# Kernel tuning notes

Hardware: AMD Instinct MI355X
Metric: run time of the kernel (lower is better)

The kernel has to match this reference:

```python
import jax, jax.numpy as jnp
import numpy as np

N_NODES = 20000
N_EDGES = 8192
UNITS = 128
NUM_GAUSSIANS = 50
CUTOFF = 8.0
GAMMA = 10.0
MIN_DIST, MAX_DIST = 0.0, 30.0


def setup_inputs() -> dict:
    key = jax.random.key(0)
    ks = jax.random.split(key, 6)
    node_features = jax.random.normal(ks[0], (N_NODES, UNITS), dtype=jnp.float32)
    edge_indices = jax.random.randint(ks[1], (2, N_EDGES), 0, N_NODES, dtype=jnp.int32)
    distances = jax.random.uniform(ks[2], (N_EDGES,), dtype=jnp.float32)
    # filter network params (Dense(units) -> swish -> Dense(units*units))
    W1 = jax.random.normal(ks[3], (NUM_GAUSSIANS, UNITS), dtype=jnp.float32) / np.sqrt(NUM_GAUSSIANS)
    b1 = jnp.zeros((UNITS,), dtype=jnp.float32)
    W2 = jax.random.normal(ks[4], (UNITS, UNITS * UNITS), dtype=jnp.float32) / np.sqrt(UNITS)
    b2 = jnp.zeros((UNITS * UNITS,), dtype=jnp.float32)
    # transform Dense(units, use_bias=False)
    Wt = jax.random.normal(ks[5], (UNITS, UNITS), dtype=jnp.float32) / np.sqrt(UNITS)
    return {"node_features": node_features, "edge_indices": edge_indices,
            "distances": distances, "W1": W1, "b1": b1, "W2": W2, "b2": b2, "Wt": Wt}


def reference(node_features, edge_indices, distances, W1, b1, W2, b2, Wt):
    n_nodes, units = node_features.shape
    # cutoff mask (multiplicative; dropped edges contribute zero to the scatter-sum,
    # equivalent to tf.boolean_mask + unsorted_segment_sum)
    mask = (distances <= CUTOFF).astype(node_features.dtype)  # [E]
    # Gaussian basis expansion
    centers = jnp.linspace(MIN_DIST, MAX_DIST, NUM_GAUSSIANS, dtype=jnp.float32)
    df = jnp.exp(-GAMMA * jnp.square(distances[:, None] - centers[None, :]))  # [E, G]
    # filter network: Dense -> swish -> Dense(units*units)
    h = jax.nn.silu(df @ W1 + b1)                    # [E, U]
    filters = (h @ W2 + b2).reshape(-1, units, units)  # [E, U, U]
    # gather source node features, transform, per-edge matvec
    src = node_features[edge_indices[0]]             # [E, U]
    transformed = src @ Wt                           # [E, U]
    filtered = jnp.einsum('eij,ej->ei', filters, transformed) * mask[:, None]  # [E, U]
    # scatter-sum to destination nodes
    messages = jax.ops.segment_sum(filtered, edge_indices[1], num_segments=n_nodes)
    return jax.nn.silu(messages)
```

## Files before the change

kernel.cpp:

```cpp
#include <hip/hip_runtime.h>
#include <hip/hip_fp16.h>


typedef _Float16 f16;
typedef __attribute__((ext_vector_type(8))) f16 f16x8;
typedef __attribute__((ext_vector_type(4))) float f32x4;
typedef __attribute__((ext_vector_type(4))) unsigned int u32x4;

#define NEDGE 8192
#define NNODE 20000
#define NG    50
#define KSTEPS 516
#define W2C_BYTES (KSTEPS * 8192)
#define HT_BYTES (64 * 132 * 128 * 2)
#define TM_BYTES (NEDGE * 128 * 2)
#define FP_BYTES ((size_t)NEDGE * 8 * 128 * 4)

#define LDS_H   0
#define LDS_TM  5120
#define LDS_TOT 37888

#define K_SRC 0
#define K_DF  16384
#define K_MSK 24576
#define K_WTC 24832
#define K_W1C 57600
#define K_TOT 73984

static __device__ __forceinline__ float fsilu(float x) { return x / (1.0f + __expf(-x)); }

static __device__ __forceinline__ void gll16(const void* g, void* l) {
  __builtin_amdgcn_global_load_lds(
      (const __attribute__((address_space(1))) unsigned int*)g,
      (__attribute__((address_space(3))) unsigned int*)l, 16, 0, 0);
}

__global__ __launch_bounds__(256) void kpre(const float* __restrict__ W2,
                                            const float* __restrict__ b2,
                                            const float* __restrict__ W1,
                                            const float* __restrict__ B1,
                                            const float* __restrict__ WT,
                                            const float* __restrict__ NF,
                                            const int*   __restrict__ EI,
                                            const float* __restrict__ DI,
                                            f16* __restrict__ w2c,
                                            f16* __restrict__ ht2,
                                            f16* __restrict__ tmo,
                                            float* __restrict__ out, int nz4) {
  __shared__ u32x4 smem_v[K_TOT / 16];
  char* smem = (char*)smem_v;
  const int bid = blockIdx.x, tid = threadIdx.x;

  if (bid < 516) {
    const int u = bid >> 2, s = bid & 3;
    const int i = tid >> 1, half = tid & 1;
    const float* src = ((u < 128) ? (W2 + (size_t)u * 16384) : b2)
                       + i * 128 + s * 32 + half * 16;
    union { f16 s16[16]; u32x4 v[2]; } pk;
#pragma unroll
    for (int q = 0; q < 4; ++q) {
      f32x4 v = *(const f32x4*)(src + q * 4);
#pragma unroll
      for (int r = 0; r < 4; ++r) pk.s16[q * 4 + r] = (f16)v[r];
    }
    const int nt = i >> 4, l15 = i & 15;
    u32x4* dst = (u32x4*)w2c + (size_t)(u * 4 + s) * 512 + nt * 64 + l15;
    dst[(half * 2 + 0) * 16] = pk.v[0];
    dst[(half * 2 + 1) * 16] = pk.v[1];
    return;
  }
  if (bid < 644) {
    const int bid2 = bid - 516;
    const int e0g = bid2 * 64;
    const int eb  = bid2 >> 1;
    const int el0 = (bid2 & 1) * 64;

#pragma unroll
    for (int q = 0; q < 8; ++q) {
      int f = q * 256 + tid;
      int lane = f & 63, nt = (f >> 6) & 7, step = f >> 9;
      int j = nt * 16 + (lane & 15);
      int u0 = step * 32 + (lane >> 4) * 8;
      union { f16 s[8]; u32x4 v; } pk;
#pragma unroll
      for (int r = 0; r < 8; ++r) pk.s[r] = (f16)WT[(u0 + r) * 128 + j];
      *(u32x4*)(smem + K_WTC + f * 16) = pk.v;
    }
#pragma unroll
    for (int q = 0; q < 4; ++q) {
      int f = q * 256 + tid;
      int lane = f & 63, nt = (f >> 6) & 7, step = f >> 9;
      int j = nt * 16 + (lane & 15);
      union { f16 s[8]; u32x4 v; } pk;
#pragma unroll
      for (int r = 0; r < 8; ++r) {
        int g = step * 32 + (lane >> 4) * 8 + r;
        float v = (g < 50) ? W1[g * 128 + j] : ((g == 63) ? B1[j] : 0.0f);
        pk.s[r] = (f16)v;
      }
      *(u32x4*)(smem + K_W1C + f * 16) = pk.v;
    }
    if (tid < 64) {
      float d = DI[e0g + tid];
      *(float*)(smem + K_MSK + tid * 4) = (d <= 8.0f) ? 1.0f : 0.0f;
    }
    {
      int e = tid >> 2, g0 = (tid & 3) * 16;
      float d = DI[e0g + e];
      union { f16 s[16]; u32x4 v[2]; } pk;
#pragma unroll
      for (int gg = 0; gg < 16; ++gg) {
        int g = g0 + gg;
        float x = d - (float)g * (30.0f / 49.0f);
        float v = (g < 50) ? __expf(-10.0f * x * x) : ((g == 63) ? 1.0f : 0.0f);
        pk.s[gg] = (f16)v;
      }
      int base = e * 128 + g0 * 2, sw = (e & 7) << 4;
      *(u32x4*)(smem + K_DF + ((base) ^ sw))      = pk.v[0];
      *(u32x4*)(smem + K_DF + ((base + 16) ^ sw)) = pk.v[1];
    }
#pragma unroll
    for (int p = 0; p < 8; ++p) {
      int e = p * 8 + (tid >> 5);
      int u0 = (tid & 31) * 4;
      int row = EI[e0g + e];
      f32x4 v = *(const f32x4*)(NF + (size_t)row * 128 + u0);
      union { f16 s[4]; unsigned long long q; } pk;
#pragma unroll
      for (int r = 0; r < 4; ++r) pk.s[r] = (f16)v[r];
      int addr = e * 256 + u0 * 2;
      *(unsigned long long*)(smem + K_SRC + (addr ^ ((e & 7) << 4))) = pk.q;
    }
    __syncthreads();

    const int w = tid >> 6, lane = tid & 63;
    const int l15 = lane & 15, g4 = lane >> 4;
    const int erow = w * 16;
    const int asw = (l15 & 7) << 4;

    f32x4 at[8], ah[8];
#pragma unroll
    for (int nt = 0; nt < 8; ++nt) {
      at[nt] = (f32x4){0.f, 0.f, 0.f, 0.f};
      ah[nt] = (f32x4){0.f, 0.f, 0.f, 0.f};
    }
#pragma unroll
    for (int step = 0; step < 4; ++step) {
      int aaddr = (erow + l15) * 256 + step * 64 + g4 * 16;
      f16x8 a = *(const f16x8*)(smem + K_SRC + (aaddr ^ asw));
#pragma unroll
      for (int nt = 0; nt < 8; ++nt) {
        f16x8 b = *(const f16x8*)(smem + K_WTC + ((step * 8 + nt) * 64 + lane) * 16);
        at[nt] = __builtin_amdgcn_mfma_f32_16x16x32_f16(a, b, at[nt], 0, 0, 0);
      }
    }
#pragma unroll
    for (int step = 0; step < 2; ++step) {
      int aaddr = (erow + l15) * 128 + step * 64 + g4 * 16;
      f16x8 a = *(const f16x8*)(smem + K_DF + (aaddr ^ asw));
#pragma unroll
      for (int nt = 0; nt < 8; ++nt) {
        f16x8 b = *(const f16x8*)(smem + K_W1C + ((step * 8 + nt) * 64 + lane) * 16);
        ah[nt] = __builtin_amdgcn_mfma_f32_16x16x32_f16(a, b, ah[nt], 0, 0, 0);
      }
    }
    const float* mk = (const float*)(smem + K_MSK);
#pragma unroll
    for (int r = 0; r < 4; ++r) {
      int el_ = erow + g4 * 4 + r;
      float m = mk[el_];
      int sw2 = (el_ & 7) << 4;
      char* rowp = (char*)tmo + (size_t)(e0g + el_) * 256;
#pragma unroll
      for (int nt = 0; nt < 8; ++nt)
        *(f16*)(rowp + (((nt * 16 + l15) * 2) ^ sw2)) = (f16)(m * at[nt][r]);
    }
#pragma unroll
    for (int r = 0; r < 4; ++r) {
      int el_ = el0 + erow + g4 * 4 + r;
#pragma unroll
      for (int nt = 0; nt < 8; ++nt) {
        int u = nt * 16 + l15;
        ht2[((size_t)eb * 132 + u) * 128 + el_] = (f16)fsilu(ah[nt][r]);
      }
    }
    if (tid < 64) ht2[((size_t)eb * 132 + 128) * 128 + el0 + tid] = (f16)1.0f;
    return;
  }
  {
    int base = (bid - 644) * 1024;
    f32x4 z = {0.f, 0.f, 0.f, 0.f};
#pragma unroll
    for (int k = 0; k < 4; ++k) {
      int i4 = base + k * 256 + tid;
      if (i4 < nz4) ((f32x4*)out)[i4] = z;
    }
  }
}

template<int MODE>
__global__ __launch_bounds__(256, 2) void k2_gemm(const f16* __restrict__ w2c,
                                                  const f16* __restrict__ ht2,
                                                  const f16* __restrict__ tm,
                                                  const int* __restrict__ EI,
                                                  float* __restrict__ fpart,
                                                  float* __restrict__ msg) {
  __shared__ u32x4 smem_v[LDS_TOT / 16];
  char* smem = (char*)smem_v;

  const int bid = blockIdx.x;
  const int c   = bid & 7;
  const int eb  = bid >> 3;
  const int e0  = eb * 128;
  const int nu  = (c == 7) ? 17 : 16;
  const int tid = threadIdx.x, w = tid >> 6, lane = tid & 63;
  const int l15 = lane & 15, g4 = lane >> 4;
  const int wm = w >> 1, wn = w & 1;

  const char* bp = (const char*)w2c + (size_t)(c * 64) * 8192 + wn * 4096 + lane * 16;
  f16x8 B0[4], B1[4];
#pragma unroll
  for (int nt = 0; nt < 4; ++nt) B0[nt] = *(const f16x8*)(bp + nt * 1024);
#pragma unroll
  for (int nt = 0; nt < 4; ++nt) B1[nt] = *(const f16x8*)(bp + 8192 + nt * 1024);

  {
    const char* tsrc = (const char*)tm + (size_t)e0 * 256 + w * 8192;
#pragma unroll
    for (int q = 0; q < 8; ++q)
      gll16(tsrc + q * 1024 + lane * 16,
            smem + LDS_TM + w * 8192 + q * 1024 + lane * 16);
  }
  if (w == 0) {
    const char* hsrc = (const char*)ht2 + ((size_t)eb * 132 + c * 16) * 256;
#pragma unroll
    for (int q = 0; q < 5; ++q)
      gll16(hsrc + q * 1024 + lane * 16, smem + LDS_H + q * 1024 + lane * 16);
  }
  __syncthreads();

  f16x8 Tall[4][4];
  {
    const int tmrow = LDS_TM + (wm * 64 + l15) * 256;
    const int colsw = (l15 & 7) << 4;
#pragma unroll
    for (int rt = 0; rt < 4; ++rt)
#pragma unroll
      for (int jc = 0; jc < 4; ++jc)
        Tall[rt][jc] = *(const f16x8*)(smem + tmrow + rt * 4096 +
                                       ((jc * 64 + g4 * 16) ^ colsw));
  }
  const __half* hbase = (const __half*)(smem + LDS_H) + wm * 64 + l15;

  __half2 hc[4], hn[4];
#pragma unroll
  for (int rt = 0; rt < 4; ++rt) hc[rt] = __half2half2(hbase[rt * 16]);

  size_t off = 2 * 8192;
  f32x4 acc[4][4];
#pragma unroll
  for (int rt = 0; rt < 4; ++rt)
#pragma unroll
    for (int nt = 0; nt < 4; ++nt) acc[rt][nt] = (f32x4){0.f, 0.f, 0.f, 0.f};

  for (int u = 0; u < nu; ++u) {
#pragma unroll
    for (int jc = 0; jc < 4; ++jc) {
      if (jc == 1) {
#pragma unroll
        for (int rt = 0; rt < 4; ++rt)
          hn[rt] = __half2half2(hbase[(u + 1) * 128 + rt * 16]);
      }
      union uf { f16x8 v; __half2 h[4]; };
      uf a[4];
#pragma unroll
      for (int rt = 0; rt < 4; ++rt) {
        uf t; t.v = Tall[rt][jc];
#pragma unroll
        for (int q = 0; q < 4; ++q) a[rt].h[q] = __hmul2(t.h[q], hc[rt]);
      }
      __builtin_amdgcn_s_setprio(1);
#pragma unroll
      for (int nt = 0; nt < 4; ++nt) {
        if ((jc & 1) == 0) {
#pragma unroll
          for (int rt = 0; rt < 4; ++rt)
            acc[rt][nt] = __builtin_amdgcn_mfma_f32_16x16x32_f16(a[rt].v, B0[nt], acc[rt][nt], 0, 0, 0);
          B0[nt] = *(const f16x8*)(bp + off + nt * 1024);
        } else {
#pragma unroll
          for (int rt = 0; rt < 4; ++rt)
            acc[rt][nt] = __builtin_amdgcn_mfma_f32_16x16x32_f16(a[rt].v, B1[nt], acc[rt][nt], 0, 0, 0);
          B1[nt] = *(const f16x8*)(bp + off + nt * 1024);
        }
      }
      __builtin_amdgcn_s_setprio(0);
      off += 8192;
    }
#pragma unroll
    for (int rt = 0; rt < 4; ++rt) hc[rt] = hn[rt];
  }

  if (MODE == 0) {
#pragma unroll
    for (int rt = 0; rt < 4; ++rt) {
#pragma unroll
      for (int r = 0; r < 4; ++r) {
        int e = e0 + wm * 64 + rt * 16 + g4 * 4 + r;
        float* prow = fpart + ((size_t)e * 8 + c) * 128 + wn * 64 + l15;
#pragma unroll
        for (int nt = 0; nt < 4; ++nt)
          prow[nt * 16] = acc[rt][nt][r];
      }
    }
  } else {
    const int* dst = EI + NEDGE;
#pragma unroll
    for (int rt = 0; rt < 4; ++rt) {
#pragma unroll
      for (int r = 0; r < 4; ++r) {
        int e = e0 + wm * 64 + rt * 16 + g4 * 4 + r;
        float* row = msg + (size_t)dst[e] * 128 + wn * 64 + l15;
#pragma unroll
        for (int nt = 0; nt < 4; ++nt)
          atomicAdd(row + nt * 16, acc[rt][nt][r]);
      }
    }
  }
}

__global__ __launch_bounds__(256) void k4_reduce(const float* __restrict__ fp,
                                                 const int* __restrict__ EI,
                                                 float* __restrict__ out) {
  int gid = blockIdx.x * 256 + threadIdx.x;
  int e  = gid >> 5;
  int i0 = (gid & 31) << 2;
  const float* ep = fp + (size_t)e * 1024 + i0;
  f32x4 s = {0.f, 0.f, 0.f, 0.f};
#pragma unroll
  for (int cc = 0; cc < 8; ++cc) {
    f32x4 v = *(const f32x4*)(ep + cc * 128);
    s[0] += v[0]; s[1] += v[1]; s[2] += v[2]; s[3] += v[3];
  }
  float* row = out + (size_t)EI[NEDGE + e] * 128 + i0;
  atomicAdd(row + 0, s[0]);
  atomicAdd(row + 1, s[1]);
  atomicAdd(row + 2, s[2]);
  atomicAdd(row + 3, s[3]);
}

__global__ __launch_bounds__(256) void k3_silu(float* __restrict__ out, int n4) {
  int idx = blockIdx.x * 256 + threadIdx.x;
  int stride = gridDim.x * 256;
  f32x4* p = (f32x4*)out;
  for (; idx < n4; idx += stride) {
    f32x4 v = p[idx];
#pragma unroll
    for (int cc = 0; cc < 4; ++cc) v[cc] = fsilu(v[cc]);
    p[idx] = v;
  }
}

extern "C" void kernel_launch(void* const* d_in, const int* in_sizes, int n_in,
                              void* d_out, int out_size, void* d_ws, size_t ws_size,
                              hipStream_t stream) {
  const float* NF = (const float*)d_in[0];
  const int*   EI = (const int*)  d_in[1];
  const float* DI = (const float*)d_in[2];
  const float* W1 = (const float*)d_in[3];
  const float* B1 = (const float*)d_in[4];
  const float* W2 = (const float*)d_in[5];
  const float* B2 = (const float*)d_in[6];
  const float* WT = (const float*)d_in[7];
  float* out = (float*)d_out;

  char* base = (char*)d_ws;
  f16*   w2c = (f16*)base;
  f16*   ht2 = (f16*)(base + W2C_BYTES);
  f16*   tmo = (f16*)(base + W2C_BYTES + HT_BYTES);
  float* fp  = (float*)(base + W2C_BYTES + HT_BYTES + TM_BYTES);
  size_t need_min  = (size_t)W2C_BYTES + HT_BYTES + TM_BYTES;
  size_t need_fast = need_min + FP_BYTES;
  if (ws_size < need_min) return;
  const bool fast = (ws_size >= need_fast);

  int nz4 = out_size / 4;
  int zb  = (nz4 + 1023) / 1024;
  kpre<<<dim3(644 + zb), dim3(256), 0, stream>>>(W2, B2, W1, B1, WT, NF, EI, DI,
                                                 w2c, ht2, tmo, out, nz4);
  if (fast) {
    k2_gemm<0><<<dim3(512),  dim3(256), 0, stream>>>(w2c, ht2, tmo, EI, fp, out);
    k4_reduce <<<dim3(1024), dim3(256), 0, stream>>>(fp, EI, out);
  } else {
    k2_gemm<1><<<dim3(512),  dim3(256), 0, stream>>>(w2c, ht2, tmo, EI, fp, out);
  }
  k3_silu<<<dim3(1024), dim3(256), 0, stream>>>(out, nz4);
}
```

Measured before the change: 82.20 us.

## Fuse reduce and silu into GEMM kernel using grid-wide atomic barriers

Merges the partial-sum reduction kernel and the final silu kernel into the GEMM kernel. Phases are separated by a software grid barrier built on an atomic counter in the workspace, and the counter is reset by the preceding kernel. This removes two kernel launches and their launch gaps. It relies on all 512 blocks being co-resident (launch bounds of 2 blocks per CU on 256 CUs), and the spin-wait barriers add synchronisation cost and a deadlock risk if residency is not met.

```diff
diff --git a/kernel.cpp b/kernel.cpp
--- a/kernel.cpp
+++ b/kernel.cpp
@@ -14,6 +14,7 @@
 #define W2C_BYTES (KSTEPS * 8192)
 #define HT_BYTES (64 * 132 * 128 * 2)
 #define TM_BYTES (NEDGE * 128 * 2)
+#define CNT_BYTES 256
 #define FP_BYTES ((size_t)NEDGE * 8 * 128 * 4)
 
 #define LDS_H   0
@@ -33,6 +34,17 @@
   __builtin_amdgcn_global_load_lds(
       (const __attribute__((address_space(1))) unsigned int*)g,
       (__attribute__((address_space(3))) unsigned int*)l, 16, 0, 0);
+}
+
+static __device__ __forceinline__ void gbar(unsigned* cnt, unsigned target) {
+  __syncthreads();
+  if (threadIdx.x == 0) {
+    __threadfence();
+    __hip_atomic_fetch_add(cnt, 1u, __ATOMIC_ACQ_REL, __HIP_MEMORY_SCOPE_AGENT);
+    while (__hip_atomic_load(cnt, __ATOMIC_ACQUIRE, __HIP_MEMORY_SCOPE_AGENT) < target)
+      __builtin_amdgcn_s_sleep(8);
+  }
+  __syncthreads();
 }
 
 __global__ __launch_bounds__(256) void kpre(const float* __restrict__ W2,
@@ -46,7 +58,8 @@
                                             f16* __restrict__ w2c,
                                             f16* __restrict__ ht2,
                                             f16* __restrict__ tmo,
-                                            float* __restrict__ out, int nz4) {
+                                            float* __restrict__ out,
+                                            unsigned* __restrict__ cnt, int nz4) {
   __shared__ u32x4 smem_v[K_TOT / 16];
   char* smem = (char*)smem_v;
   const int bid = blockIdx.x, tid = threadIdx.x;
@@ -188,6 +201,7 @@
     return;
   }
   {
+    if (bid == 644 && tid == 0) *cnt = 0u;
     int base = (bid - 644) * 1024;
     f32x4 z = {0.f, 0.f, 0.f, 0.f};
 #pragma unroll
@@ -199,12 +213,13 @@
 }
 
 template<int MODE>
-__global__ __launch_bounds__(256, 2) void k2_gemm(const f16* __restrict__ w2c,
-                                                  const f16* __restrict__ ht2,
-                                                  const f16* __restrict__ tm,
-                                                  const int* __restrict__ EI,
-                                                  float* __restrict__ fpart,
-                                                  float* __restrict__ msg) {
+__global__ __launch_bounds__(256, 2) void k2f(const f16* __restrict__ w2c,
+                                              const f16* __restrict__ ht2,
+                                              const f16* __restrict__ tm,
+                                              const int* __restrict__ EI,
+                                              float* __restrict__ fpart,
+                                              float* __restrict__ out,
+                                              unsigned* __restrict__ cnt, int nz4) {
   __shared__ u32x4 smem_v[LDS_TOT / 16];
   char* smem = (char*)smem_v;
 
@@ -320,44 +335,49 @@
 #pragma unroll
       for (int r = 0; r < 4; ++r) {
         int e = e0 + wm * 64 + rt * 16 + g4 * 4 + r;
-        float* row = msg + (size_t)dst[e] * 128 + wn * 64 + l15;
+        float* row = out + (size_t)dst[e] * 128 + wn * 64 + l15;
 #pragma unroll
         for (int nt = 0; nt < 4; ++nt)
           atomicAdd(row + nt * 16, acc[rt][nt][r]);
       }
     }
   }
-}
-
-__global__ __launch_bounds__(256) void k4_reduce(const float* __restrict__ fp,
-                                                 const int* __restrict__ EI,
-                                                 float* __restrict__ out) {
-  int gid = blockIdx.x * 256 + threadIdx.x;
-  int e  = gid >> 5;
-  int i0 = (gid & 31) << 2;
-  const float* ep = fp + (size_t)e * 1024 + i0;
-  f32x4 s = {0.f, 0.f, 0.f, 0.f};
-#pragma unroll
-  for (int cc = 0; cc < 8; ++cc) {
-    f32x4 v = *(const f32x4*)(ep + cc * 128);
-    s[0] += v[0]; s[1] += v[1]; s[2] += v[2]; s[3] += v[3];
-  }
-  float* row = out + (size_t)EI[NEDGE + e] * 128 + i0;
-  atomicAdd(row + 0, s[0]);
-  atomicAdd(row + 1, s[1]);
-  atomicAdd(row + 2, s[2]);
-  atomicAdd(row + 3, s[3]);
-}
-
-__global__ __launch_bounds__(256) void k3_silu(float* __restrict__ out, int n4) {
-  int idx = blockIdx.x * 256 + threadIdx.x;
-  int stride = gridDim.x * 256;
-  f32x4* p = (f32x4*)out;
-  for (; idx < n4; idx += stride) {
-    f32x4 v = p[idx];
-#pragma unroll
-    for (int cc = 0; cc < 4; ++cc) v[cc] = fsilu(v[cc]);
-    p[idx] = v;
+
+  if (MODE == 0) {
+    gbar(cnt, 512);
+    const int* dst = EI + NEDGE;
+#pragma unroll
+    for (int it = 0; it < 2; ++it) {
+      int gid = it * 131072 + bid * 256 + tid;
+      int e  = gid >> 5;
+      int i0 = (gid & 31) << 2;
+      const float* ep = fpart + (size_t)e * 1024 + i0;
+      f32x4 s = {0.f, 0.f, 0.f, 0.f};
+#pragma unroll
+      for (int cc = 0; cc < 8; ++cc) {
+        f32x4 v = *(const f32x4*)(ep + cc * 128);
+        s[0] += v[0]; s[1] += v[1]; s[2] += v[2]; s[3] += v[3];
+      }
+      float* row = out + (size_t)dst[e] * 128 + i0;
+      atomicAdd(row + 0, s[0]);
+      atomicAdd(row + 1, s[1]);
+      atomicAdd(row + 2, s[2]);
+      atomicAdd(row + 3, s[3]);
+    }
+    gbar(cnt, 1024);
+  } else {
+    gbar(cnt, 512);
+  }
+
+  {
+    int idx = bid * 256 + tid;
+    f32x4* p = (f32x4*)out;
+    for (; idx < nz4; idx += 512 * 256) {
+      f32x4 v = p[idx];
+#pragma unroll
+      for (int cc = 0; cc < 4; ++cc) v[cc] = fsilu(v[cc]);
+      p[idx] = v;
+    }
   }
 }
 
@@ -375,11 +395,12 @@
   float* out = (float*)d_out;
 
   char* base = (char*)d_ws;
-  f16*   w2c = (f16*)base;
-  f16*   ht2 = (f16*)(base + W2C_BYTES);
-  f16*   tmo = (f16*)(base + W2C_BYTES + HT_BYTES);
-  float* fp  = (float*)(base + W2C_BYTES + HT_BYTES + TM_BYTES);
-  size_t need_min  = (size_t)W2C_BYTES + HT_BYTES + TM_BYTES;
+  f16*      w2c = (f16*)base;
+  f16*      ht2 = (f16*)(base + W2C_BYTES);
+  f16*      tmo = (f16*)(base + W2C_BYTES + HT_BYTES);
+  unsigned* cnt = (unsigned*)(base + W2C_BYTES + HT_BYTES + TM_BYTES);
+  float*    fp  = (float*)(base + W2C_BYTES + HT_BYTES + TM_BYTES + CNT_BYTES);
+  size_t need_min  = (size_t)W2C_BYTES + HT_BYTES + TM_BYTES + CNT_BYTES;
   size_t need_fast = need_min + FP_BYTES;
   if (ws_size < need_min) return;
   const bool fast = (ws_size >= need_fast);
@@ -387,12 +408,10 @@
   int nz4 = out_size / 4;
   int zb  = (nz4 + 1023) / 1024;
   kpre<<<dim3(644 + zb), dim3(256), 0, stream>>>(W2, B2, W1, B1, WT, NF, EI, DI,
-                                                 w2c, ht2, tmo, out, nz4);
+                                                 w2c, ht2, tmo, out, cnt, nz4);
   if (fast) {
-    k2_gemm<0><<<dim3(512),  dim3(256), 0, stream>>>(w2c, ht2, tmo, EI, fp, out);
-    k4_reduce <<<dim3(1024), dim3(256), 0, stream>>>(fp, EI, out);
+    k2f<0><<<dim3(512), dim3(256), 0, stream>>>(w2c, ht2, tmo, EI, fp, out, cnt, nz4);
   } else {
-    k2_gemm<1><<<dim3(512),  dim3(256), 0, stream>>>(w2c, ht2, tmo, EI, fp, out);
-  }
-  k3_silu<<<dim3(1024), dim3(256), 0, stream>>>(out, nz4);
+    k2f<1><<<dim3(512), dim3(256), 0, stream>>>(w2c, ht2, tmo, EI, fp, out, cnt, nz4);
+  }
 }
```

Result: slower. 230.0 us (+179.7%).
